# Optimization experiments

Measured on AMD Instinct MI355X. Metric: run time of the kernel, lower is better.

Reference implementation:

```python
import jax, jax.numpy as jnp
import numpy as np

B, C, N = 8, 256, 4096

def setup_inputs() -> dict:
    key = jax.random.key(0)
    k1, k2, k3 = jax.random.split(key, 3)
    pts_feat = jax.random.normal(k1, (B, C, N), dtype=jnp.float32)
    # Conv1d(channels, channels, 1, bias=False) weight is [C_out, C_in, 1] -> store as [C_out, C_in]
    scale = 1.0 / np.sqrt(C)
    Wq = jax.random.uniform(k2, (C, C), dtype=jnp.float32, minval=-scale, maxval=scale)
    Wk = jax.random.uniform(k3, (C, C), dtype=jnp.float32, minval=-scale, maxval=scale)
    return {"pts_feat": pts_feat, "Wq": Wq, "Wk": Wk}

def reference(pts_feat, Wq, Wk):
    # 1x1 conv == channel-wise matmul. x_q: [B, N, C], x_k: [B, C, N]
    x_q = jnp.einsum('bcn,dc->bnd', pts_feat, Wq)
    x_k = jnp.einsum('bcn,dc->bdn', pts_feat, Wk)
    logits = jnp.einsum('bnc,bcm->bnm', x_q, x_k)          # [B, N, N]
    attn = jax.nn.softmax(logits, axis=-1)
    attn = attn / (1e-8 + attn.sum(axis=-1, keepdims=True))
    # torch.einsum('bnn,bnc->bnc', attn, feat) takes the DIAGONAL of attn
    # and scales each point's raw feature vector by it (no contraction).
    diag = jnp.diagonal(attn, axis1=1, axis2=2)            # [B, N]
    x_attn = pts_feat * diag[:, None, :]                   # [B, C, N]
    return x_attn
```

## Files before the change

kernel.cpp:

```cpp
#include <hip/hip_runtime.h>
#include <hip/hip_bf16.h>
#include <cstdint>

#define B_ 8
#define C_ 256
#define N_ 4096

typedef __bf16 bf16;
typedef __bf16 bf16x8 __attribute__((ext_vector_type(8)));
typedef float f32x4 __attribute__((ext_vector_type(4)));
typedef unsigned int u32;

__device__ __forceinline__ void async_ld16(const void* g, void* l) {
  __builtin_amdgcn_global_load_lds(
      (const __attribute__((address_space(1))) void*)g,
      (__attribute__((address_space(3))) void*)l, 16, 0, 0);
}

__device__ __forceinline__ float bh2f(unsigned short u) {
  union { u32 i; float f; } x; x.i = ((u32)u) << 16; return x.f;
}
__device__ __forceinline__ unsigned short f2bh(float f) {
  union { float f; u32 i; } x; x.f = f;
  u32 i = x.i + 0x7fffu + ((x.i >> 16) & 1u);
  return (unsigned short)(i >> 16);
}

__device__ __forceinline__ bool wave_sniff_fp32(const unsigned short* p) {
  int l = threadIdx.x & 63;
  unsigned short u = p[2 * l];
  int e = (u >> 7) & 0xff;
  unsigned long long m = __ballot(e >= 112 && e <= 142);
  return __popcll(m) < 32;
}

__global__ __launch_bounds__(256) void k_pre(const void* __restrict__ Wqv,
                                             const void* __restrict__ Wkv,
                                             const void* __restrict__ Fv,
                                             unsigned short* __restrict__ Mt,
                                             unsigned short* __restrict__ Ft) {
  __shared__ float wkcol[C_];
  __shared__ unsigned short tile[64 * 66];
  int bid = blockIdx.x;
  int t = threadIdx.x;
  if (bid < 256) {
    bool fq = wave_sniff_fp32((const unsigned short*)Wqv);
    bool fk = wave_sniff_fp32((const unsigned short*)Wkv);
    int d = bid, c = t;
    if (fk)
      wkcol[c] = ((const float*)Wkv)[c * C_ + d];
    else
      wkcol[c] = bh2f(((const unsigned short*)Wkv)[c * C_ + d]);
    __syncthreads();
    float acc = 0.f;
    if (fq) {
      for (int e0 = 0; e0 < C_; e0 += 16) {
        float wq[16];
#pragma unroll
        for (int j = 0; j < 16; ++j) wq[j] = ((const float*)Wqv)[(e0 + j) * C_ + c];
#pragma unroll
        for (int j = 0; j < 16; ++j) acc += wkcol[e0 + j] * wq[j];
      }
    } else {
      for (int e0 = 0; e0 < C_; e0 += 16) {
        float wq[16];
#pragma unroll
        for (int j = 0; j < 16; ++j) wq[j] = bh2f(((const unsigned short*)Wqv)[(e0 + j) * C_ + c]);
#pragma unroll
        for (int j = 0; j < 16; ++j) acc += wkcol[e0 + j] * wq[j];
      }
    }
    Mt[(size_t)d * C_ + c] = f2bh(acc);
    return;
  }
  bool f32 = wave_sniff_fp32((const unsigned short*)Fv);
  int id = bid - 256;
  int n0 = (id & 63) * 64, c0 = ((id >> 6) & 3) * 64, b = id >> 8;
#pragma unroll
  for (int p = 0; p < 2; ++p) {
    int c = (t >> 3) + 32 * p;
    int n = (t & 7) * 8;
    size_t off = (size_t)(b * C_ + c0 + c) * N_ + n0 + n;
    unsigned short vals[8];
    if (f32) {
      const float* src = (const float*)Fv + off;
      float4 v0 = *(const float4*)(src);
      float4 v1 = *(const float4*)(src + 4);
      vals[0] = f2bh(v0.x); vals[1] = f2bh(v0.y); vals[2] = f2bh(v0.z); vals[3] = f2bh(v0.w);
      vals[4] = f2bh(v1.x); vals[5] = f2bh(v1.y); vals[6] = f2bh(v1.z); vals[7] = f2bh(v1.w);
    } else {
      uint4 v = *(const uint4*)((const unsigned short*)Fv + off);
      vals[0] = (unsigned short)(v.x & 0xffffu); vals[1] = (unsigned short)(v.x >> 16);
      vals[2] = (unsigned short)(v.y & 0xffffu); vals[3] = (unsigned short)(v.y >> 16);
      vals[4] = (unsigned short)(v.z & 0xffffu); vals[5] = (unsigned short)(v.z >> 16);
      vals[6] = (unsigned short)(v.w & 0xffffu); vals[7] = (unsigned short)(v.w >> 16);
    }
#pragma unroll
    for (int s = 0; s < 8; ++s) tile[c * 66 + n + s] = vals[s];
  }
  __syncthreads();
#pragma unroll
  for (int p = 0; p < 2; ++p) {
    int n = (t >> 3) + 32 * p;
    int c8 = (t & 7) * 8;
    u32 o[4];
#pragma unroll
    for (int k = 0; k < 4; ++k) {
      unsigned short lo = tile[(c8 + 2 * k) * 66 + n];
      unsigned short hi = tile[(c8 + 2 * k + 1) * 66 + n];
      o[k] = ((u32)hi << 16) | lo;
    }
    uint4 ov; ov.x = o[0]; ov.y = o[1]; ov.z = o[2]; ov.w = o[3];
    *(uint4*)(Ft + ((size_t)(b * N_ + n0 + n) * C_ + c0 + c8)) = ov;
  }
}

__global__ __launch_bounds__(256, 4) void k_proj(const bf16* __restrict__ Ft,
                                                 const bf16* __restrict__ Mt,
                                                 bf16* __restrict__ G) {
  __shared__ bf16 As[8 * 64 * 32];
  int n0 = blockIdx.x * 64;
  int b = blockIdx.y;
  int d0 = blockIdx.z * 128;
  int t = threadIdx.x, w = t >> 6, l = t & 63;
  int lr = l & 15, lq = l >> 4;
  int wn = w * 32;
  const size_t fbase = (size_t)b * N_ * C_;

  int srow = t >> 2;
  int schunk = ((t & 3) ^ ((t >> 3) & 3)) * 8;
#pragma unroll
  for (int kc = 0; kc < 8; ++kc)
    async_ld16(Ft + fbase + (size_t)(n0 + srow) * C_ + kc * 32 + schunk,
               As + kc * 2048 + t * 8);

  bf16x8 bb[2][8];
#pragma unroll
  for (int j = 0; j < 2; ++j)
#pragma unroll
    for (int kc = 0; kc < 8; ++kc)
      bb[j][kc] = *(const bf16x8*)(Mt + (size_t)(d0 + wn + 16 * j + lr) * C_ + kc * 32 + lq * 8);

  __syncthreads();
  int rchunk = (lq ^ ((lr >> 1) & 3)) * 8;
  f32x4 acc[4][2] = {};
#pragma unroll
  for (int kc = 0; kc < 8; ++kc) {
#pragma unroll
    for (int i = 0; i < 4; ++i) {
      bf16x8 a = *(const bf16x8*)(As + kc * 2048 + (16 * i + lr) * 32 + rchunk);
#pragma unroll
      for (int j = 0; j < 2; ++j)
        acc[i][j] = __builtin_amdgcn_mfma_f32_16x16x32_bf16(a, bb[j][kc], acc[i][j], 0, 0, 0);
    }
  }
  __syncthreads();
  unsigned short* Cs = (unsigned short*)As;
#pragma unroll
  for (int i = 0; i < 4; ++i)
#pragma unroll
    for (int j = 0; j < 2; ++j)
#pragma unroll
      for (int r = 0; r < 4; ++r)
        Cs[(16 * i + lq * 4 + r) * 136 + wn + 16 * j + lr] = f2bh(acc[i][j][r]);
  __syncthreads();
#pragma unroll
  for (int p = 0; p < 4; ++p) {
    int idx = p * 256 + t;
    int row = idx >> 4, c8 = idx & 15;
    uint4 v = *(const uint4*)(Cs + row * 136 + c8 * 8);
    *(uint4*)(G + fbase + (size_t)(n0 + row) * C_ + d0 + c8 * 8) = v;
  }
}

__global__ __launch_bounds__(256, 4) void k_attn(const bf16* __restrict__ G,
                                                 const bf16* __restrict__ Ft,
                                                 float* __restrict__ snn,
                                                 float* __restrict__ lsum) {
  __shared__ bf16 Ks[8 * 64 * 32];
  int bid = blockIdx.x;
  int b = bid & 7, q = (bid >> 3) & 3, ntile = bid >> 5;
  int n0 = ntile * 128;
  int t = threadIdx.x, w = t >> 6, l = t & 63;
  int lr = l & 15, lq = l >> 4;
  int wrow = w * 32;
  const size_t gbase = (size_t)b * N_ * C_;

  bf16x8 a[2][8];
#pragma unroll
  for (int i = 0; i < 2; ++i)
#pragma unroll
    for (int kc = 0; kc < 8; ++kc)
      a[i][kc] = *(const bf16x8*)(G + gbase + (size_t)(n0 + wrow + 16 * i + lr) * C_ + kc * 32 + lq * 8);

  float part[8];
#pragma unroll
  for (int s = 0; s < 8; ++s) part[s] = 0.f;

  int m_base = q * 1024;
  bool has_diag = (q == (ntile >> 3));
  int d0 = (ntile & 7) * 2;

  int srow = t >> 2;
  int schunk = ((t & 3) ^ ((t >> 3) & 3)) * 8;
  int rchunk = (lq ^ ((lr >> 1) & 3)) * 8;

  for (int it = 0; it < 16; ++it) {
    int m0 = m_base + it * 64;
    __syncthreads();
#pragma unroll
    for (int kc = 0; kc < 8; ++kc)
      async_ld16(Ft + gbase + (size_t)(m0 + srow) * C_ + kc * 32 + schunk,
                 Ks + kc * 2048 + t * 8);
    __syncthreads();
    f32x4 acc[2][4] = {};
#pragma unroll
    for (int kc = 0; kc < 8; ++kc) {
      bf16x8 bb[4];
#pragma unroll
      for (int j = 0; j < 4; ++j)
        bb[j] = *(const bf16x8*)(Ks + kc * 2048 + (16 * j + lr) * 32 + rchunk);
#pragma unroll
      for (int i = 0; i < 2; ++i)
#pragma unroll
        for (int j = 0; j < 4; ++j)
          acc[i][j] = __builtin_amdgcn_mfma_f32_16x16x32_bf16(a[i][kc], bb[j], acc[i][j], 0, 0, 0);
    }
    bool dit = has_diag && ((it >> 1) == (ntile & 7));
#pragma unroll
    for (int i = 0; i < 2; ++i)
#pragma unroll
      for (int j = 0; j < 4; ++j)
#pragma unroll
        for (int r = 0; r < 4; ++r) {
          float e = __expf(acc[i][j][r]);
          part[i * 4 + r] += e;
          if (dit) {
            int rloc = wrow + 16 * i + lq * 4 + r;
            int cloc = 16 * j + lr;
            if ((it - d0) * 64 + cloc == rloc) snn[b * N_ + n0 + rloc] = e;
          }
        }
  }

#pragma unroll
  for (int s = 0; s < 8; ++s) {
    float v = part[s];
    v += __shfl_xor(v, 1);
    v += __shfl_xor(v, 2);
    v += __shfl_xor(v, 4);
    v += __shfl_xor(v, 8);
    part[s] = v;
  }
  if (lr == 0) {
#pragma unroll
    for (int i = 0; i < 2; ++i)
#pragma unroll
      for (int r = 0; r < 4; ++r)
        lsum[((size_t)q * B_ + b) * N_ + n0 + wrow + 16 * i + lq * 4 + r] = part[i * 4 + r];
  }
}

__global__ __launch_bounds__(256) void k_scale(const void* __restrict__ Fv,
                                               const float* __restrict__ snn,
                                               const float* __restrict__ lsum,
                                               void* __restrict__ Outv) {
  bool f32 = wave_sniff_fp32((const unsigned short*)Fv);
  int g = blockIdx.x * 256 + threadIdx.x;
  size_t base = (size_t)g * 8;
  int n = (int)(base & (N_ - 1));
  int b = (int)(base >> 20);
  float4 s0 = *(const float4*)(snn + (size_t)b * N_ + n);
  float4 s1 = *(const float4*)(snn + (size_t)b * N_ + n + 4);
  float ls[8];
#pragma unroll
  for (int k = 0; k < 8; ++k) ls[k] = 0.f;
#pragma unroll
  for (int p = 0; p < 4; ++p) {
    float4 l0 = *(const float4*)(lsum + ((size_t)p * B_ + b) * N_ + n);
    float4 l1 = *(const float4*)(lsum + ((size_t)p * B_ + b) * N_ + n + 4);
    ls[0] += l0.x; ls[1] += l0.y; ls[2] += l0.z; ls[3] += l0.w;
    ls[4] += l1.x; ls[5] += l1.y; ls[6] += l1.z; ls[7] += l1.w;
  }
  const float c1 = 1.0f + 1e-8f;
  float dd[8];
  dd[0] = s0.x / (ls[0] * c1); dd[1] = s0.y / (ls[1] * c1);
  dd[2] = s0.z / (ls[2] * c1); dd[3] = s0.w / (ls[3] * c1);
  dd[4] = s1.x / (ls[4] * c1); dd[5] = s1.y / (ls[5] * c1);
  dd[6] = s1.z / (ls[6] * c1); dd[7] = s1.w / (ls[7] * c1);
  if (f32) {
    const float* F = (const float*)Fv + base;
    float* O = (float*)Outv + base;
    float4 a0 = *(const float4*)(F);
    float4 a1 = *(const float4*)(F + 4);
    float4 o0, o1;
    o0.x = a0.x * dd[0]; o0.y = a0.y * dd[1]; o0.z = a0.z * dd[2]; o0.w = a0.w * dd[3];
    o1.x = a1.x * dd[4]; o1.y = a1.y * dd[5]; o1.z = a1.z * dd[6]; o1.w = a1.w * dd[7];
    *(float4*)(O) = o0;
    *(float4*)(O + 4) = o1;
  } else {
    uint4 v = *(const uint4*)((const unsigned short*)Fv + base);
    u32 vv[4] = {v.x, v.y, v.z, v.w};
    u32 o[4];
#pragma unroll
    for (int k = 0; k < 4; ++k) {
      float lo = bh2f((unsigned short)(vv[k] & 0xffffu)) * dd[2 * k];
      float hi = bh2f((unsigned short)(vv[k] >> 16)) * dd[2 * k + 1];
      o[k] = ((u32)f2bh(hi) << 16) | f2bh(lo);
    }
    uint4 ov; ov.x = o[0]; ov.y = o[1]; ov.z = o[2]; ov.w = o[3];
    *(uint4*)((unsigned short*)Outv + base) = ov;
  }
}

extern "C" void kernel_launch(void* const* d_in, const int* in_sizes, int n_in,
                              void* d_out, int out_size, void* d_ws, size_t ws_size,
                              hipStream_t stream) {
  (void)in_sizes; (void)n_in; (void)out_size; (void)ws_size;
  const void* F = d_in[0];
  const void* Wq = d_in[1];
  const void* Wk = d_in[2];
  char* ws = (char*)d_ws;
  bf16* Ft = (bf16*)(ws);
  bf16* G = (bf16*)(ws + (16u << 20));
  char* tail = ws + (32u << 20);
  float* snn = (float*)(tail);
  float* lsum = (float*)(tail + 131072);
  bf16* Mt = (bf16*)(tail + 131072 + 524288);

  k_pre<<<256 + 2048, 256, 0, stream>>>(Wq, Wk, F, (unsigned short*)Mt, (unsigned short*)Ft);
  k_proj<<<dim3(N_ / 64, B_, 2), 256, 0, stream>>>(Ft, Mt, G);
  k_attn<<<1024, 256, 0, stream>>>(G, Ft, snn, lsum);
  k_scale<<<(B_ * C_ * N_ / 8) / 256, 256, 0, stream>>>(F, snn, lsum, d_out);
}
```

Measured before the change: 183.4 us.

## Double-buffer K tiles in attention kernel with smaller 32-row tiles

The k_attn loop now stages 32-row K tiles into two LDS buffers and prefetches the next tile with async global-to-LDS loads while MFMAs run on the current one. A single wait plus barrier per iteration replaces the two syncthreads around each load. The tile is halved from 64 to 32 rows so the double buffer fits in the same LDS budget, and the diagonal-extraction indexing is adjusted to match. The intent is to hide global load latency behind compute, at the cost of twice as many iterations and less MFMA work per barrier.

```diff
diff --git a/kernel.cpp b/kernel.cpp
--- a/kernel.cpp
+++ b/kernel.cpp
@@ -177,7 +177,7 @@
                                                  const bf16* __restrict__ Ft,
                                                  float* __restrict__ snn,
                                                  float* __restrict__ lsum) {
-  __shared__ bf16 Ks[8 * 64 * 32];
+  __shared__ bf16 Ks[2][32 * 256];
   int bid = blockIdx.x;
   int b = bid & 7, q = (bid >> 3) & 3, ntile = bid >> 5;
   int n0 = ntile * 128;
@@ -199,38 +199,51 @@
 
   int m_base = q * 1024;
   bool has_diag = (q == (ntile >> 3));
-  int d0 = (ntile & 7) * 2;
-
-  int srow = t >> 2;
-  int schunk = ((t & 3) ^ ((t >> 3) & 3)) * 8;
+  int dbase = (ntile & 7) * 4;
+
+  int soff[4];
+#pragma unroll
+  for (int p = 0; p < 4; ++p) {
+    int flat = p * 256 + t;
+    int kc = flat >> 7;
+    int r = (flat >> 2) & 31;
+    int col8 = flat & 3;
+    soff[p] = r * C_ + kc * 32 + ((col8 ^ ((r >> 1) & 3)) * 8);
+  }
   int rchunk = (lq ^ ((lr >> 1) & 3)) * 8;
 
-  for (int it = 0; it < 16; ++it) {
-    int m0 = m_base + it * 64;
-    __syncthreads();
-#pragma unroll
-    for (int kc = 0; kc < 8; ++kc)
-      async_ld16(Ft + gbase + (size_t)(m0 + srow) * C_ + kc * 32 + schunk,
-                 Ks + kc * 2048 + t * 8);
-    __syncthreads();
-    f32x4 acc[2][4] = {};
+#pragma unroll
+  for (int p = 0; p < 4; ++p)
+    async_ld16(Ft + gbase + (size_t)m_base * C_ + soff[p],
+               (bf16*)Ks + (p * 256 + t) * 8);
+  asm volatile("s_waitcnt vmcnt(0)" ::: "memory");
+  __builtin_amdgcn_s_barrier();
+
+  for (int it = 0; it < 32; ++it) {
+    int cur = it & 1;
+    if (it < 31) {
+      int m0 = m_base + (it + 1) * 32;
+#pragma unroll
+      for (int p = 0; p < 4; ++p)
+        async_ld16(Ft + gbase + (size_t)m0 * C_ + soff[p],
+                   (bf16*)Ks + (cur ^ 1) * 8192 + (p * 256 + t) * 8);
+    }
+    const bf16* ks = (const bf16*)Ks + cur * 8192;
+    f32x4 acc[2][2] = {};
 #pragma unroll
     for (int kc = 0; kc < 8; ++kc) {
-      bf16x8 bb[4];
-#pragma unroll
-      for (int j = 0; j < 4; ++j)
-        bb[j] = *(const bf16x8*)(Ks + kc * 2048 + (16 * j + lr) * 32 + rchunk);
-#pragma unroll
-      for (int i = 0; i < 2; ++i)
-#pragma unroll
-        for (int j = 0; j < 4; ++j)
-          acc[i][j] = __builtin_amdgcn_mfma_f32_16x16x32_bf16(a[i][kc], bb[j], acc[i][j], 0, 0, 0);
-    }
-    bool dit = has_diag && ((it >> 1) == (ntile & 7));
+      bf16x8 b0 = *(const bf16x8*)(ks + kc * 1024 + lr * 32 + rchunk);
+      bf16x8 b1 = *(const bf16x8*)(ks + kc * 1024 + (16 + lr) * 32 + rchunk);
+      acc[0][0] = __builtin_amdgcn_mfma_f32_16x16x32_bf16(a[0][kc], b0, acc[0][0], 0, 0, 0);
+      acc[1][0] = __builtin_amdgcn_mfma_f32_16x16x32_bf16(a[1][kc], b0, acc[1][0], 0, 0, 0);
+      acc[0][1] = __builtin_amdgcn_mfma_f32_16x16x32_bf16(a[0][kc], b1, acc[0][1], 0, 0, 0);
+      acc[1][1] = __builtin_amdgcn_mfma_f32_16x16x32_bf16(a[1][kc], b1, acc[1][1], 0, 0, 0);
+    }
+    bool dit = has_diag && ((it >> 2) == (ntile & 7));
 #pragma unroll
     for (int i = 0; i < 2; ++i)
 #pragma unroll
-      for (int j = 0; j < 4; ++j)
+      for (int j = 0; j < 2; ++j)
 #pragma unroll
         for (int r = 0; r < 4; ++r) {
           float e = __expf(acc[i][j][r]);
@@ -238,9 +251,13 @@
           if (dit) {
             int rloc = wrow + 16 * i + lq * 4 + r;
             int cloc = 16 * j + lr;
-            if ((it - d0) * 64 + cloc == rloc) snn[b * N_ + n0 + rloc] = e;
+            if ((it - dbase) * 32 + cloc == rloc) snn[b * N_ + n0 + rloc] = e;
           }
         }
+    if (it < 31) {
+      asm volatile("s_waitcnt vmcnt(0)" ::: "memory");
+      __builtin_amdgcn_s_barrier();
+    }
   }
 
 #pragma unroll
```

Measured after the change: 177.0 us. 3.5% less time.
